# Optimization experiments

Measured on AMD Instinct MI355X. Metric: run time of the kernel, lower is better.

## Reference

```python
import jax, jax.numpy as jnp
import numpy as np

# Static config (matches init_kwargs / input_specs)
B, D, H, W, C = 1, 16, 56, 56, 128
NH = 4
WS = (8, 7, 7)            # window size (d, h, w)
SS = (4, 3, 3)            # shift size = window // 2
HID = 4 * C
L = WS[0] * WS[1] * WS[2]  # 392 tokens per window
SCALE = (C // NH) ** -0.5
TABLE = (2 * WS[0] - 1) * (2 * WS[1] - 1) * (2 * WS[2] - 1)  # 2535


def _rel_index_np(wd, wh, ww):
    # Faithful to VideoSwinWindowAttention.get_relative_position_index
    yy, zz, xx = np.meshgrid(np.arange(ww), np.arange(wd), np.arange(wh))  # 'xy'
    coords = np.stack([zz, yy, xx], axis=0).reshape(3, -1)
    rc = coords[:, :, None] - coords[:, None, :]
    rc = rc.transpose(1, 2, 0)
    z = (rc[:, :, 0] + wd - 1) * (2 * wh - 1) * (2 * ww - 1)
    x = (rc[:, :, 1] + wh - 1) * (2 * ww - 1)
    y = rc[:, :, 2] + ww - 1
    return (z + x + y).astype(np.int32)  # (L, L)


def _partition_np(x, ws):
    b, d, h, w, c = x.shape
    x = x.reshape(b, d // ws[0], ws[0], h // ws[1], ws[1], w // ws[2], ws[2], c)
    x = x.transpose(0, 1, 3, 5, 2, 4, 6, 7)
    return x.reshape(-1, ws[0] * ws[1] * ws[2], c)


def _compute_mask_np(d, h, w, ws, ss):
    img = np.zeros((1, d, h, w, 1))
    cnt = 0
    for ds in (slice(-ws[0]), slice(-ws[0], -ss[0]), slice(-ss[0], None)):
        for hs in (slice(-ws[1]), slice(-ws[1], -ss[1]), slice(-ss[1], None)):
            for wsl in (slice(-ws[2]), slice(-ws[2], -ss[2]), slice(-ss[2], None)):
                img[:, ds, hs, wsl, :] = cnt
                cnt += 1
    mw = _partition_np(img, ws)[..., 0]  # (nW, L)
    am = mw[:, None, :] - mw[:, :, None]
    return np.where(am != 0, -100.0, 0.0).astype(np.float32)  # (nW, L, L)


REL_INDEX = jnp.asarray(_rel_index_np(*WS))            # (L, L) int32
ATTN_MASK = jnp.asarray(_compute_mask_np(D, H, W, WS, SS))  # (nW, L, L)


def window_partition(x, ws):
    b, d, h, w, c = x.shape
    x = x.reshape(b, d // ws[0], ws[0], h // ws[1], ws[1], w // ws[2], ws[2], c)
    x = x.transpose(0, 1, 3, 5, 2, 4, 6, 7)
    return x.reshape(-1, ws[0] * ws[1] * ws[2], c)


def window_reverse(win, ws, b, d, h, w):
    x = win.reshape(b, d // ws[0], h // ws[1], w // ws[2], ws[0], ws[1], ws[2], -1)
    x = x.transpose(0, 1, 4, 2, 5, 3, 6, 7)
    return x.reshape(b, d, h, w, -1)


def layer_norm(x, g, b, eps=1e-5):
    m = jnp.mean(x, axis=-1, keepdims=True)
    v = jnp.mean(jnp.square(x - m), axis=-1, keepdims=True)
    return (x - m) * jax.lax.rsqrt(v + eps) * g + b


def window_attention(xw, qkv_w, qkv_b, rpb, proj_w, proj_b, mask):
    bn = xw.shape[0]
    qkv = (xw @ qkv_w + qkv_b).reshape(bn, L, 3, NH, C // NH)
    q = qkv[:, :, 0].transpose(0, 2, 1, 3) * SCALE  # (bn, NH, L, hd)
    k = qkv[:, :, 1].transpose(0, 2, 1, 3)
    v = qkv[:, :, 2].transpose(0, 2, 1, 3)
    attn = jnp.einsum('bhld,bhmd->bhlm', q, k)
    bias = rpb[REL_INDEX.reshape(-1)].reshape(L, L, NH).transpose(2, 0, 1)
    attn = attn + bias[None]
    if mask is not None:
        nw = mask.shape[0]
        attn = attn.reshape(bn // nw, nw, NH, L, L) + mask[None, :, None]
        attn = attn.reshape(bn, NH, L, L)
    attn = jax.nn.softmax(attn, axis=-1)
    out = jnp.einsum('bhlm,bhmd->bhld', attn, v)
    out = out.transpose(0, 2, 1, 3).reshape(bn, L, C)
    return out @ proj_w + proj_b


def swin_block(x, p, shift, mask):
    shortcut = x
    x = layer_norm(x, p[0], p[1])
    if shift is not None:
        x = jnp.roll(x, (-shift[0], -shift[1], -shift[2]), axis=(1, 2, 3))
    xw = window_partition(x, WS)
    xw = window_attention(xw, p[2], p[3], p[4], p[5], p[6], mask)
    x = window_reverse(xw, WS, B, D, H, W)
    if shift is not None:
        x = jnp.roll(x, shift, axis=(1, 2, 3))
    x = shortcut + x
    y = layer_norm(x, p[7], p[8])
    y = jax.nn.gelu(y @ p[9] + p[10], approximate=False) @ p[11] + p[12]
    return x + y


def setup_inputs() -> dict:
    key = jax.random.key(0)
    ks = jax.random.split(key, 8)
    s = 0.02
    return {
        'x': jax.random.normal(ks[0], (B, D, H, W, C), jnp.float32),
        'ln1_g': jnp.ones((2, C), jnp.float32),
        'ln1_b': jnp.zeros((2, C), jnp.float32),
        'qkv_w': jax.random.normal(ks[1], (2, C, 3 * C), jnp.float32) * s,
        'qkv_b': jnp.zeros((2, 3 * C), jnp.float32),
        'rpb': jax.random.normal(ks[2], (2, TABLE, NH), jnp.float32) * s,
        'proj_w': jax.random.normal(ks[3], (2, C, C), jnp.float32) * s,
        'proj_b': jnp.zeros((2, C), jnp.float32),
        'ln2_g': jnp.ones((2, C), jnp.float32),
        'ln2_b': jnp.zeros((2, C), jnp.float32),
        'fc1_w': jax.random.normal(ks[4], (2, C, HID), jnp.float32) * s,
        'fc1_b': jnp.zeros((2, HID), jnp.float32),
        'fc2_w': jax.random.normal(ks[5], (2, HID, C), jnp.float32) * s,
        'fc2_b': jnp.zeros((2, C), jnp.float32),
    }


def reference(x, ln1_g, ln1_b, qkv_w, qkv_b, rpb, proj_w, proj_b,
              ln2_g, ln2_b, fc1_w, fc1_b, fc2_w, fc2_b):
    # Block 0: W-MSA (no shift, no mask). Block 1: SW-MSA (shift + mask).
    for i, (shift, mask) in enumerate(((None, None), (SS, ATTN_MASK))):
        p = (ln1_g[i], ln1_b[i], qkv_w[i], qkv_b[i], rpb[i], proj_w[i],
             proj_b[i], ln2_g[i], ln2_b[i], fc1_w[i], fc1_b[i], fc2_w[i], fc2_b[i])
        x = swin_block(x, p, shift, mask)
    return x
```

## Files before the change

kernel.cpp:

```cpp
#include <hip/hip_runtime.h>
#include <hip/hip_bf16.h>
#include <math.h>


#define NTOK 50176
#define CC   128
#define LL   392
#define NWIN 128
#define NHEAD 4
#define HDIM 32
#define QKSCALE 0.17677669529663687f
#define LOG2E   1.4426950408889634f

#define KOFF    0
#define VOFF    12544
#define POFF    25088
#define LDS_U16 33280

#define KTILE   12544

#define KADDR(row, g) (((row) << 5) + ((((g) ^ ((row) & 3) ^ (((row) >> 2) & 3))) << 3))
#define VADDR(d, k) (VOFF + (d)*392 + (k))

#define BM_PER_HEAD (13*392*16)
#define BM_TOTAL    (8*4*BM_PER_HEAD)

typedef unsigned short u16;
typedef unsigned int   u32;
typedef unsigned long long u64;
typedef __attribute__((ext_vector_type(8))) short short8;
typedef __attribute__((ext_vector_type(4))) float f32x4;
typedef __attribute__((ext_vector_type(2))) unsigned int u32x2;
typedef __attribute__((ext_vector_type(4))) unsigned int u32x4;

#define GLDS(gp, lp) __builtin_amdgcn_global_load_lds( \
    (const __attribute__((address_space(1))) void*)(gp), \
    (__attribute__((address_space(3))) void*)(lp), 16, 0, 0)

__device__ __forceinline__ float b2f_lo(u32 u){ return __uint_as_float(u<<16); }
__device__ __forceinline__ float b2f_hi(u32 u){ return __uint_as_float(u & 0xffff0000u); }
__device__ __forceinline__ u16 f2b(float f){
  __hip_bfloat16 h = __float2bfloat16(f);
  return *reinterpret_cast<u16*>(&h);
}
__device__ __forceinline__ u32 cvtpk(float lo, float hi){
  u32 r; asm("v_cvt_pk_bf16_f32 %0, %1, %2" : "=v"(r) : "v"(lo), "v"(hi)); return r;
}

__device__ __forceinline__ int row_to_pos(int r, int shifted){
  int w = r / LL, t = r - w*LL;
  int wd = w >> 6, wh = (w >> 3) & 7, ww = w & 7;
  int td = t / 49, rem = t - td*49, th = rem / 7, tw = rem - th*7;
  int d = wd*8 + td, h = wh*7 + th, x = ww*7 + tw;
  if (shifted){ d = (d+4)&15; h += 3; if (h>=56) h-=56; x += 3; if (x>=56) x-=56; }
  return (d*56 + h)*56 + x;
}

__device__ __forceinline__ int pos_to_row_sh(int p){
  int d = p / 3136, rem = p - d*3136, h = rem / 56, x = rem - h*56;
  d = (d + 12) & 15; h -= 3; if (h < 0) h += 56; x -= 3; if (x < 0) x += 56;
  int wd = d >> 3, td = d & 7;
  int wh = h / 7, th = h - wh*7, ww = x / 7, tw = x - ww*7;
  return (wd*64 + wh*8 + ww)*LL + td*49 + th*7 + tw;
}

__global__ __launch_bounds__(256) void ln_kernel(
    const float* __restrict__ xf, const float* __restrict__ g,
    const float* __restrict__ b, u16* __restrict__ out, int do_map, int shifted)
{
  int wave = threadIdx.x >> 6, lane = threadIdx.x & 63;
  int r = blockIdx.x*4 + wave;
  int pos = do_map ? row_to_pos(r, shifted) : r;
  long src = (long)pos * CC;
  float v0 = xf[src+lane], v1 = xf[src+64+lane];
  float s = v0+v1, ss = v0*v0 + v1*v1;
  #pragma unroll
  for (int o=32; o>0; o>>=1){ s += __shfl_xor(s,o); ss += __shfl_xor(ss,o); }
  float mean = s*(1.f/CC);
  float var  = ss*(1.f/CC) - mean*mean;
  float rstd = rsqrtf(var + 1e-5f);
  long dst = (long)r*CC;
  out[dst + lane]      = f2b((v0-mean)*rstd*g[lane]    + b[lane]);
  out[dst + 64 + lane] = f2b((v1-mean)*rstd*g[64+lane] + b[64+lane]);
}

__global__ __launch_bounds__(256) void wtall_kernel(
    const float* __restrict__ qkvw, const float* __restrict__ projw,
    const float* __restrict__ fc1w, const float* __restrict__ fc2w,
    u16* __restrict__ wts)
{
  int t = blockIdx.x*256 + threadIdx.x;
  int blk = t / 196608, r = t - blk*196608;
  const float* in; int Kd, Nd, off;
  if (r < 49152)      { in = qkvw + (size_t)blk*49152; Kd = 128; Nd = 384; off = r; }
  else if (r < 65536) { in = projw + (size_t)blk*16384; Kd = 128; Nd = 128; off = r - 49152; }
  else if (r < 131072){ in = fc1w + (size_t)blk*65536;  Kd = 128; Nd = 512; off = r - 65536; }
  else                { in = fc2w + (size_t)blk*65536;  Kd = 512; Nd = 128; off = r - 131072; }
  int n = off / Kd, k = off - n*Kd;
  wts[t] = f2b(in[k*Nd + n]);
}

__global__ __launch_bounds__(256) void biasm_kernel(
    const float* __restrict__ rpb, u32* __restrict__ bm, int total)
{
  int t = blockIdx.x*256 + threadIdx.x;
  if (t >= total) return;
  int jj = t & 15; int rest = t >> 4;
  int i  = rest % 392; rest /= 392;
  int s  = rest % 13;  rest /= 13;
  int h  = rest & 3;   int cls = rest >> 2;
  int tdi=i/49, rmi=i-tdi*49, thi=rmi/7, twi=rmi-thi*7;
  u32 pack = 0;
  #pragma unroll
  for (int half=0; half<2; half++){
    int j = s*32 + jj + half*16;
    float v = -1e30f;
    if (j < LL){
      int tdj=j/49, rmj=j-tdj*49, thj=rmj/7, twj=rmj-thj*7;
      int idx = (tdi-tdj)*169 + (thi-thj)*13 + (twi-twj) + 1267;
      v = rpb[idx*NHEAD + h];
      bool neq = ((cls&4) && ((tdi<4) != (tdj<4)))
              || ((cls&2) && ((thi<4) != (thj<4)))
              || ((cls&1) && ((twi<4) != (twj<4)));
      if (neq) v -= 100.f;
      v *= LOG2E;
    }
    pack |= ((u32)f2b(v)) << (16*half);
  }
  bm[t] = pack;
}

template<int KD, int EPI, int LNF, int NW>
__global__ __launch_bounds__(NW*64) void mm_kernel(
    const u16* __restrict__ A, const u16* __restrict__ Wt, int ldw,
    const float* __restrict__ bias, u16* __restrict__ OutB, int ldo,
    float* __restrict__ OutF, const float* __restrict__ Res,
    const float* __restrict__ lng, const float* __restrict__ lnb,
    float scaleq, int shifted, int use_bias)
{
  constexpr int NCH  = NW/2;
  constexpr int COLW = 128/NCH;
  constexpr int CT   = COLW/16;
  constexpr bool SWAPG = (EPI == 0);

  __shared__ __align__(16) u16 As[2*128*32];
  __shared__ __align__(16) u16 Bs[2*128*32];
  const int tid = threadIdx.x, lane = tid & 63, wv = tid >> 6;
  const int quad = lane >> 4, l15 = lane & 15;
  const int rh = wv / NCH, ch = wv % NCH;
  const int r0 = (SWAPG ? blockIdx.y : blockIdx.x) * 128;
  const int n0 = (SWAPG ? blockIdx.x : blockIdx.y) * 128;
  const int srow = lane >> 2, spart = (lane & 3) * 8;
  const int nkt = KD/32;

  f32x4 acc[4][CT] = {};

  auto stage = [&](int kt, int bo){
    const int k0 = kt*32;
    #pragma unroll
    for (int t=0;t<8/NW;t++){
      const int rowbase = (wv*(8/NW) + t)*16;
      GLDS(&A [(long)(r0 + rowbase + srow)*KD  + k0 + spart], &As[bo + rowbase*32]);
      GLDS(&Wt[(long)(n0 + rowbase + srow)*ldw + k0 + spart], &Bs[bo + rowbase*32]);
    }
  };
  auto compute = [&](int bo){
    short8 af[4], bf[CT];
    #pragma unroll
    for (int rt=0;rt<4;rt++)
      af[rt] = *reinterpret_cast<const short8*>(&As[bo + (rh*64 + rt*16 + l15)*32 + quad*8]);
    #pragma unroll
    for (int ct=0;ct<CT;ct++)
      bf[ct] = *reinterpret_cast<const short8*>(&Bs[bo + (ch*COLW + ct*16 + l15)*32 + quad*8]);
    #pragma unroll
    for (int rt=0;rt<4;rt++)
      #pragma unroll
      for (int ct=0;ct<CT;ct++)
        acc[rt][ct] = __builtin_amdgcn_mfma_f32_16x16x32_bf16(af[rt], bf[ct], acc[rt][ct], 0,0,0);
  };

  stage(0, 0);
  asm volatile("s_waitcnt vmcnt(0)" ::: "memory");
  __builtin_amdgcn_s_barrier();

  int cur = 0;
  for (int kt = 0; kt < nkt-1; kt++){
    stage(kt+1, 4096 - cur);
    compute(cur);
    asm volatile("s_waitcnt vmcnt(0)" ::: "memory");
    __builtin_amdgcn_s_barrier();
    cur = 4096 - cur;
  }
  compute(cur);

  if (EPI == 0){
    const int y = n0 >> 7;
    if (y == 0){
      #pragma unroll
      for (int rt=0;rt<4;rt++)
        #pragma unroll
        for (int rr=0;rr<4;rr++){
          const int row_g = r0 + rh*64 + rt*16 + quad*4 + rr;
          #pragma unroll
          for (int ct=0;ct<CT;ct++){
            const int c = ch*COLW + ct*16 + l15;
            float v = (acc[rt][ct][rr] + bias[c]) * scaleq;
            OutB[(long)row_g*128 + c] = f2b(v);
          }
        }
    } else if (y == 1){
      u16* Kreg = OutB + (size_t)NTOK*128;
      #pragma unroll
      for (int rt=0;rt<4;rt++)
        #pragma unroll
        for (int rr=0;rr<4;rr++){
          const int row_g = r0 + rh*64 + rt*16 + quad*4 + rr;
          const int wi = row_g / 392, key = row_g - wi*392;
          #pragma unroll
          for (int ct=0;ct<CT;ct++){
            const int c = ch*COLW + ct*16 + l15;
            const int hd = c >> 5, d = c & 31;
            float v = acc[rt][ct][rr] + bias[128 + c];
            Kreg[(size_t)(wi*4 + hd)*KTILE + KADDR(key, d>>3) + (d&7)] = f2b(v);
          }
        }
    } else {
      u16* Vreg = OutB + (size_t)NTOK*256;
      #pragma unroll
      for (int rt=0;rt<4;rt++){
        const int rbase = r0 + rh*64 + rt*16 + quad*4;
        const int wi = rbase / 392, key0 = rbase - wi*392;
        #pragma unroll
        for (int ct=0;ct<CT;ct++){
          const int c = ch*COLW + ct*16 + l15;
          const int hd = c >> 5, d = c & 31;
          const float bb = bias[256 + c];
          u32 lo = cvtpk(acc[rt][ct][0] + bb, acc[rt][ct][1] + bb);
          u32 hi = cvtpk(acc[rt][ct][2] + bb, acc[rt][ct][3] + bb);
          u64 pk = (u64)lo | ((u64)hi << 32);
          *reinterpret_cast<u64*>(&Vreg[(size_t)(wi*4 + hd)*KTILE + (size_t)d*392 + key0]) = pk;
        }
      }
    }
  } else if (LNF == 0){
    #pragma unroll
    for (int rt=0;rt<4;rt++){
      #pragma unroll
      for (int rr=0;rr<4;rr++){
        const int row_g = r0 + rh*64 + rt*16 + quad*4 + rr;
        long pos = 0;
        if (EPI == 2) pos = (long)row_to_pos(row_g, shifted) * CC;
        #pragma unroll
        for (int ct=0;ct<CT;ct++){
          const int col_g = n0 + ch*COLW + ct*16 + l15;
          float v = acc[rt][ct][rr];
          if (EPI == 1){
            v += bias[col_g];
            v = 0.5f*v*(1.f + erff(v*0.70710678118654752f));
            OutB[(long)row_g*ldo + col_g] = f2b(v);
          } else if (EPI == 2){
            OutF[pos + col_g] = Res[pos + col_g] + v + bias[col_g];
          } else {
            float o = OutF[(long)row_g*CC + col_g] + v;
            if (use_bias) o += bias[col_g];
            OutF[(long)row_g*CC + col_g] = o;
          }
        }
      }
    }
  } else {
    float* red = (float*)As;
    int pose[4][4];
    #pragma unroll
    for (int rt=0;rt<4;rt++){
      #pragma unroll
      for (int rr=0;rr<4;rr++){
        const int row_g = r0 + rh*64 + rt*16 + quad*4 + rr;
        int pos = (EPI == 2) ? row_to_pos(row_g, shifted) : row_g;
        pose[rt][rr] = pos;
        long pb = (long)pos * CC;
        float s = 0.f, ss = 0.f;
        #pragma unroll
        for (int ct=0;ct<CT;ct++){
          const int col_g = n0 + ch*COLW + ct*16 + l15;
          float v = acc[rt][ct][rr];
          float o;
          if (EPI == 2) o = Res[pb + col_g] + v + bias[col_g];
          else { o = OutF[pb + col_g] + v; if (use_bias) o += bias[col_g]; }
          OutF[pb + col_g] = o;
          acc[rt][ct][rr] = o;
          s += o; ss += o*o;
        }
        #pragma unroll
        for (int off=1; off<16; off<<=1){
          s  += __shfl_xor(s,  off);
          ss += __shfl_xor(ss, off);
        }
        if (l15 == 0){
          int rl = rh*64 + rt*16 + quad*4 + rr;
          red[rl*(2*NCH) + ch*2]     = s;
          red[rl*(2*NCH) + ch*2 + 1] = ss;
        }
      }
    }
    __syncthreads();
    #pragma unroll
    for (int rt=0;rt<4;rt++){
      #pragma unroll
      for (int rr=0;rr<4;rr++){
        const int rl = rh*64 + rt*16 + quad*4 + rr;
        float st = 0.f, sst = 0.f;
        #pragma unroll
        for (int j=0;j<NCH;j++){
          st  += red[rl*(2*NCH) + j*2];
          sst += red[rl*(2*NCH) + j*2 + 1];
        }
        float mean = st*(1.f/128.f);
        float var  = sst*(1.f/128.f) - mean*mean;
        float rstd = rsqrtf(var + 1e-5f);
        long oidx;
        if (LNF == 1) oidx = (long)pose[rt][rr] * CC;
        else          oidx = (long)pos_to_row_sh(pose[rt][rr]) * CC;
        #pragma unroll
        for (int ct=0;ct<CT;ct++){
          const int col_g = n0 + ch*COLW + ct*16 + l15;
          float val = (acc[rt][ct][rr] - mean)*rstd*lng[col_g] + lnb[col_g];
          OutB[oidx + col_g] = f2b(val);
        }
      }
    }
  }
}

__global__ __launch_bounds__(512, 4) void attn_kernel(
    const u16* __restrict__ qkv, const u32* __restrict__ bm,
    u16* __restrict__ out, int shifted)
{
  __shared__ __align__(16) u16 lds[LDS_U16];

  const int w = blockIdx.x >> 2, head = blockIdx.x & 3;
  const int tid = threadIdx.x, lane = tid & 63, wave = tid >> 6;
  const int quad = lane >> 4, l15 = lane & 15;
  const int wd = w>>6, wh = (w>>3)&7, ww = w&7;
  const int cls = shifted ? (((wd!=0)?4:0) | ((wh==7)?2:0) | ((ww==7)?1:0)) : 0;
  const u32* __restrict__ bmh = bm + (size_t)(cls*NHEAD + head)*BM_PER_HEAD;
  const int pbase = POFF + wave*1024;
  const int swz = l15 & 7;
  const int prow = pbase + l15*64;
  const int q2 = quad >> 1, qh = (quad & 1) << 2;

  {
    const u16* Kg = qkv + (size_t)NTOK*128 + (size_t)(w*4+head)*KTILE;
    const u16* Vg = qkv + (size_t)NTOK*256 + (size_t)(w*4+head)*KTILE;
    #pragma unroll
    for (int n = 0; n < 3; n++){
      GLDS(Kg + n*4096 + wave*512 + (lane<<3), &lds[KOFF + n*4096 + wave*512]);
      GLDS(Vg + n*4096 + wave*512 + (lane<<3), &lds[VOFF + n*4096 + wave*512]);
    }
    if (tid < 32){
      GLDS(Kg + 12288 + (lane<<3), &lds[KOFF + 12288]);
      GLDS(Vg + 12288 + (lane<<3), &lds[VOFF + 12288]);
    }
  }
  __syncthreads();

  for (int qt = wave; qt < 25; qt += 8){
    int iq = qt*16 + l15; if (iq > LL-1) iq = LL-1;
    short8 qf = *reinterpret_cast<const short8*>(
        &qkv[((size_t)(w*LL + iq))*128 + head*HDIM + quad*8]);

    float ls = 0.f;
    f32x4 oc0 = {0.f,0.f,0.f,0.f}, oc1 = {0.f,0.f,0.f,0.f};

    const int bmrow = iq*16 + quad*4;
    u32x4 bmA = *reinterpret_cast<const u32x4*>(&bmh[bmrow]);
    u32x4 bmB = *reinterpret_cast<const u32x4*>(&bmh[392*16 + bmrow]);
    short8 kf0 = *reinterpret_cast<const short8*>(&lds[KOFF + KADDR(     l15, quad)]);
    short8 kf1 = *reinterpret_cast<const short8*>(&lds[KOFF + KADDR(16 + l15, quad)]);
    short8 kf2 = *reinterpret_cast<const short8*>(&lds[KOFF + KADDR(32 + l15, quad)]);
    short8 kf3 = *reinterpret_cast<const short8*>(&lds[KOFF + KADDR(48 + l15, quad)]);

    for (int it = 0; it < 6; it++){
      const int kb = it*64;
      u32x4 bmAn = {}, bmBn = {};
      short8 kn0 = {}, kn1 = {}, kn2 = {}, kn3 = {};
      if (it < 5){
        bmAn = *reinterpret_cast<const u32x4*>(&bmh[(2*it+2)*392*16 + bmrow]);
        bmBn = *reinterpret_cast<const u32x4*>(&bmh[(2*it+3)*392*16 + bmrow]);
        kn0 = *reinterpret_cast<const short8*>(&lds[KOFF + KADDR(kb + 64 + l15, quad)]);
        kn1 = *reinterpret_cast<const short8*>(&lds[KOFF + KADDR(kb + 80 + l15, quad)]);
        kn2 = *reinterpret_cast<const short8*>(&lds[KOFF + KADDR(kb + 96 + l15, quad)]);
        kn3 = *reinterpret_cast<const short8*>(&lds[KOFF + KADDR(kb +112 + l15, quad)]);
      } else {
        bmAn = *reinterpret_cast<const u32x4*>(&bmh[12*392*16 + bmrow]);
        kn0 = *reinterpret_cast<const short8*>(&lds[KOFF + KADDR(384 + (l15 & 7), quad)]);
        kn1 = kn0;
      }

      f32x4 z = {0.f,0.f,0.f,0.f};
      __builtin_amdgcn_s_setprio(1);
      f32x4 c0 = __builtin_amdgcn_mfma_f32_16x16x32_bf16(kf0, qf, z, 0,0,0);
      f32x4 c1 = __builtin_amdgcn_mfma_f32_16x16x32_bf16(kf1, qf, z, 0,0,0);
      f32x4 c2 = __builtin_amdgcn_mfma_f32_16x16x32_bf16(kf2, qf, z, 0,0,0);
      f32x4 c3 = __builtin_amdgcn_mfma_f32_16x16x32_bf16(kf3, qf, z, 0,0,0);
      __builtin_amdgcn_s_setprio(0);

      float p0[4], p1[4], p2[4], p3[4];
      #pragma unroll
      for (int r=0;r<4;r++){
        p0[r] = exp2f(c0[r] + b2f_lo(bmA[r]));
        p1[r] = exp2f(c1[r] + b2f_hi(bmA[r]));
        p2[r] = exp2f(c2[r] + b2f_lo(bmB[r]));
        p3[r] = exp2f(c3[r] + b2f_hi(bmB[r]));
        ls += (p0[r] + p1[r]) + (p2[r] + p3[r]);
      }

      u32x2 w0, w1, w2, w3;
      w0.x = cvtpk(p0[0], p0[1]); w0.y = cvtpk(p0[2], p0[3]);
      w1.x = cvtpk(p1[0], p1[1]); w1.y = cvtpk(p1[2], p1[3]);
      w2.x = cvtpk(p2[0], p2[1]); w2.y = cvtpk(p2[2], p2[3]);
      w3.x = cvtpk(p3[0], p3[1]); w3.y = cvtpk(p3[2], p3[3]);
      *reinterpret_cast<u32x2*>(&lds[prow + (((0 + q2) ^ swz) << 3) + qh]) = w0;
      *reinterpret_cast<u32x2*>(&lds[prow + (((2 + q2) ^ swz) << 3) + qh]) = w1;
      *reinterpret_cast<u32x2*>(&lds[prow + (((4 + q2) ^ swz) << 3) + qh]) = w2;
      *reinterpret_cast<u32x2*>(&lds[prow + (((6 + q2) ^ swz) << 3) + qh]) = w3;

      short8 pa0 = *reinterpret_cast<const short8*>(&lds[prow + (((quad    ) ^ swz) << 3)]);
      short8 pa1 = *reinterpret_cast<const short8*>(&lds[prow + (((quad + 4) ^ swz) << 3)]);
      short8 vb00 = *reinterpret_cast<const short8*>(&lds[VADDR(     l15, kb      + quad*8)]);
      short8 vb01 = *reinterpret_cast<const short8*>(&lds[VADDR(16 + l15, kb      + quad*8)]);
      short8 vb10 = *reinterpret_cast<const short8*>(&lds[VADDR(     l15, kb + 32 + quad*8)]);
      short8 vb11 = *reinterpret_cast<const short8*>(&lds[VADDR(16 + l15, kb + 32 + quad*8)]);
      __builtin_amdgcn_s_setprio(1);
      oc0 = __builtin_amdgcn_mfma_f32_16x16x32_bf16(pa0, vb00, oc0, 0,0,0);
      oc1 = __builtin_amdgcn_mfma_f32_16x16x32_bf16(pa0, vb01, oc1, 0,0,0);
      oc0 = __builtin_amdgcn_mfma_f32_16x16x32_bf16(pa1, vb10, oc0, 0,0,0);
      oc1 = __builtin_amdgcn_mfma_f32_16x16x32_bf16(pa1, vb11, oc1, 0,0,0);
      __builtin_amdgcn_s_setprio(0);

      bmA = bmAn; bmB = bmBn;
      kf0 = kn0; kf1 = kn1; kf2 = kn2; kf3 = kn3;
    }

    {
      f32x4 z = {0.f,0.f,0.f,0.f};
      f32x4 c0 = __builtin_amdgcn_mfma_f32_16x16x32_bf16(kf0, qf, z, 0,0,0);
      f32x4 c1 = __builtin_amdgcn_mfma_f32_16x16x32_bf16(kf1, qf, z, 0,0,0);
      float p0[4], p1[4];
      #pragma unroll
      for (int r=0;r<4;r++){
        p0[r] = exp2f(c0[r] + b2f_lo(bmA[r]));
        p1[r] = exp2f(c1[r] + b2f_hi(bmA[r]));
        ls += p0[r] + p1[r];
      }
      u32x2 w0, w1;
      w0.x = cvtpk(p0[0], p0[1]); w0.y = cvtpk(p0[2], p0[3]);
      w1.x = cvtpk(p1[0], p1[1]); w1.y = cvtpk(p1[2], p1[3]);
      *reinterpret_cast<u32x2*>(&lds[prow + (((0 + q2) ^ swz) << 3) + qh]) = w0;
      *reinterpret_cast<u32x2*>(&lds[prow + (((2 + q2) ^ swz) << 3) + qh]) = w1;
      short8 pa0 = *reinterpret_cast<const short8*>(&lds[prow + ((quad ^ swz) << 3)]);
      short8 vb0 = *reinterpret_cast<const short8*>(&lds[VADDR(     l15, 384)]);
      short8 vb1 = *reinterpret_cast<const short8*>(&lds[VADDR(16 + l15, 384)]);
      oc0 = __builtin_amdgcn_mfma_f32_16x16x32_bf16(pa0, vb0, oc0, 0,0,0);
      oc1 = __builtin_amdgcn_mfma_f32_16x16x32_bf16(pa0, vb1, oc1, 0,0,0);
    }

    ls += __shfl_xor(ls, 16);
    ls += __shfl_xor(ls, 32);
    float inv = 1.f / ls;
    #pragma unroll
    for (int r=0;r<4;r++){
      float invr = __shfl(inv, quad*4 + r);
      int i = qt*16 + quad*4 + r;
      if (i < LL){
        long o = ((long)(w*LL + i))*CC + head*HDIM;
        out[o + l15]      = f2b(oc0[r]*invr);
        out[o + 16 + l15] = f2b(oc1[r]*invr);
      }
    }
  }
}

extern "C" void kernel_launch(void* const* d_in, const int* in_sizes, int n_in,
                              void* d_out, int out_size, void* d_ws, size_t ws_size,
                              hipStream_t stream)
{
  const float* x     = (const float*)d_in[0];
  const float* ln1g  = (const float*)d_in[1];
  const float* ln1b  = (const float*)d_in[2];
  const float* qkvw  = (const float*)d_in[3];
  const float* qkvb  = (const float*)d_in[4];
  const float* rpb   = (const float*)d_in[5];
  const float* projw = (const float*)d_in[6];
  const float* projb = (const float*)d_in[7];
  const float* ln2g  = (const float*)d_in[8];
  const float* ln2b  = (const float*)d_in[9];
  const float* fc1w  = (const float*)d_in[10];
  const float* fc1b  = (const float*)d_in[11];
  const float* fc2w  = (const float*)d_in[12];
  const float* fc2b  = (const float*)d_in[13];
  float* outf = (float*)d_out;

  u16* buf1 = (u16*)d_ws;
  u16* bufq = buf1 + (size_t)NTOK*CC;
  u16* ln2o = bufq + (size_t)NTOK*256;
  u16* hid  = bufq + (size_t)NTOK*384;
  u16* wts  = hid  + (size_t)NTOK*512;
  u32* bm   = (u32*)(wts + 393216);

  wtall_kernel<<<1536, 256, 0, stream>>>(qkvw, projw, fc1w, fc2w, wts);

  for (int blk = 0; blk < 2; ++blk){
    const int sh = blk;
    const float* resid = (blk==0) ? x : outf;
    u16* wb = wts + (size_t)blk*196608;

    const int bmtot = (blk==0) ? 4*BM_PER_HEAD : BM_TOTAL;
    biasm_kernel<<<(bmtot+255)/256, 256, 0, stream>>>(
        rpb + (size_t)blk*2535*NHEAD, bm, bmtot);
    if (blk == 0)
      ln_kernel<<<NTOK/4, 256, 0, stream>>>(resid,
          ln1g, ln1b, buf1, 1, 0);
    mm_kernel<128,0,0,4><<<dim3(3,392), 256, 0, stream>>>(
        buf1, wb, 128, qkvb + blk*384, bufq, 128,
        nullptr, nullptr, nullptr, nullptr, QKSCALE*LOG2E, 0, 0);
    attn_kernel<<<NWIN*NHEAD, 512, 0, stream>>>(bufq, bm, buf1, sh);
    mm_kernel<128,2,1,8><<<dim3(392,1), 512, 0, stream>>>(
        buf1, wb+49152, 128, projb + blk*CC, ln2o, 0,
        outf, resid, ln2g + blk*CC, ln2b + blk*CC, 1.f, sh, 0);
    mm_kernel<128,1,0,8><<<dim3(392,4), 512, 0, stream>>>(
        ln2o, wb + 65536, 128,
        fc1b + blk*512, hid, 512,
        nullptr, nullptr, nullptr, nullptr, 1.f, 0, 0);
    if (blk == 0){
      mm_kernel<512,3,2,8><<<dim3(392,1), 512, 0, stream>>>(
          hid, wb + 131072, 512,
          fc2b, buf1, 0,
          outf, nullptr, ln1g + CC, ln1b + CC, 1.f, 0, 1);
    } else {
      mm_kernel<512,3,0,8><<<dim3(392,1), 512, 0, stream>>>(
          hid, wb + 131072, 512,
          fc2b + CC, nullptr, 0,
          outf, nullptr, nullptr, nullptr, 1.f, 0, 1);
    }
  }
}
```

Before: 380.8 us.

## Deepen GEMM prefetch pipeline and fold attention bias into MFMA accumulator

The GEMM kernel now takes a template buffer count (3 or 4) and prefetches up to two K-tiles ahead. It waits with partial vmcnt values, so later tiles' global-to-LDS loads keep running while the current tile is computed, instead of waiting for all loads at every step. In the attention kernel, the combined bias/mask values now seed the QK^T MFMA accumulator rather than being added before exp2, which removes the per-element adds. The price is more LDS per GEMM block, which may lower occupancy, and a little more register setup for the bias vectors.

```diff
diff --git a/kernel.cpp b/kernel.cpp
--- a/kernel.cpp
+++ b/kernel.cpp
@@ -130,7 +130,7 @@
   bm[t] = pack;
 }
 
-template<int KD, int EPI, int LNF, int NW>
+template<int KD, int EPI, int LNF, int NW, int NBUF>
 __global__ __launch_bounds__(NW*64) void mm_kernel(
     const u16* __restrict__ A, const u16* __restrict__ Wt, int ldw,
     const float* __restrict__ bias, u16* __restrict__ OutB, int ldo,
@@ -142,9 +142,11 @@
   constexpr int COLW = 128/NCH;
   constexpr int CT   = COLW/16;
   constexpr bool SWAPG = (EPI == 0);
-
-  __shared__ __align__(16) u16 As[2*128*32];
-  __shared__ __align__(16) u16 Bs[2*128*32];
+  constexpr int LPS = 16/NW;
+  constexpr int LA  = NBUF - 2;
+
+  __shared__ __align__(16) u16 As[NBUF*128*32];
+  __shared__ __align__(16) u16 Bs[NBUF*128*32];
   const int tid = threadIdx.x, lane = tid & 63, wv = tid >> 6;
   const int quad = lane >> 4, l15 = lane & 15;
   const int rh = wv / NCH, ch = wv % NCH;
@@ -155,7 +157,8 @@
 
   f32x4 acc[4][CT] = {};
 
-  auto stage = [&](int kt, int bo){
+  auto stage = [&](int kt){
+    const int bo = (kt % NBUF) * 4096;
     const int k0 = kt*32;
     #pragma unroll
     for (int t=0;t<8/NW;t++){
@@ -164,7 +167,8 @@
       GLDS(&Wt[(long)(n0 + rowbase + srow)*ldw + k0 + spart], &Bs[bo + rowbase*32]);
     }
   };
-  auto compute = [&](int bo){
+  auto compute = [&](int kt){
+    const int bo = (kt % NBUF) * 4096;
     short8 af[4], bf[CT];
     #pragma unroll
     for (int rt=0;rt<4;rt++)
@@ -179,19 +183,21 @@
         acc[rt][ct] = __builtin_amdgcn_mfma_f32_16x16x32_bf16(af[rt], bf[ct], acc[rt][ct], 0,0,0);
   };
 
-  stage(0, 0);
-  asm volatile("s_waitcnt vmcnt(0)" ::: "memory");
-  __builtin_amdgcn_s_barrier();
-
-  int cur = 0;
-  for (int kt = 0; kt < nkt-1; kt++){
-    stage(kt+1, 4096 - cur);
-    compute(cur);
-    asm volatile("s_waitcnt vmcnt(0)" ::: "memory");
+  #pragma unroll
+  for (int p = 0; p < LA; p++) stage(p);
+
+  for (int kt = 0; kt < nkt; kt++){
+    if (kt + LA < nkt) stage(kt + LA);
+    const int rem = nkt - 1 - kt;
+    const int ahead = rem < LA ? rem : LA;
+    const int allow = ahead * LPS;
+    if (allow == 0)      asm volatile("s_waitcnt vmcnt(0)" ::: "memory");
+    else if (allow == 2) asm volatile("s_waitcnt vmcnt(2)" ::: "memory");
+    else if (allow == 4) asm volatile("s_waitcnt vmcnt(4)" ::: "memory");
+    else                 asm volatile("s_waitcnt vmcnt(8)" ::: "memory");
     __builtin_amdgcn_s_barrier();
-    cur = 4096 - cur;
+    compute(kt);
   }
-  compute(cur);
 
   if (EPI == 0){
     const int y = n0 >> 7;
@@ -397,21 +403,24 @@
         kn1 = kn0;
       }
 
-      f32x4 z = {0.f,0.f,0.f,0.f};
+      f32x4 cb0 = {b2f_lo(bmA[0]), b2f_lo(bmA[1]), b2f_lo(bmA[2]), b2f_lo(bmA[3])};
+      f32x4 cb1 = {b2f_hi(bmA[0]), b2f_hi(bmA[1]), b2f_hi(bmA[2]), b2f_hi(bmA[3])};
+      f32x4 cb2 = {b2f_lo(bmB[0]), b2f_lo(bmB[1]), b2f_lo(bmB[2]), b2f_lo(bmB[3])};
+      f32x4 cb3 = {b2f_hi(bmB[0]), b2f_hi(bmB[1]), b2f_hi(bmB[2]), b2f_hi(bmB[3])};
       __builtin_amdgcn_s_setprio(1);
-      f32x4 c0 = __builtin_amdgcn_mfma_f32_16x16x32_bf16(kf0, qf, z, 0,0,0);
-      f32x4 c1 = __builtin_amdgcn_mfma_f32_16x16x32_bf16(kf1, qf, z, 0,0,0);
-      f32x4 c2 = __builtin_amdgcn_mfma_f32_16x16x32_bf16(kf2, qf, z, 0,0,0);
-      f32x4 c3 = __builtin_amdgcn_mfma_f32_16x16x32_bf16(kf3, qf, z, 0,0,0);
+      f32x4 c0 = __builtin_amdgcn_mfma_f32_16x16x32_bf16(kf0, qf, cb0, 0,0,0);
+      f32x4 c1 = __builtin_amdgcn_mfma_f32_16x16x32_bf16(kf1, qf, cb1, 0,0,0);
+      f32x4 c2 = __builtin_amdgcn_mfma_f32_16x16x32_bf16(kf2, qf, cb2, 0,0,0);
+      f32x4 c3 = __builtin_amdgcn_mfma_f32_16x16x32_bf16(kf3, qf, cb3, 0,0,0);
       __builtin_amdgcn_s_setprio(0);
 
       float p0[4], p1[4], p2[4], p3[4];
       #pragma unroll
       for (int r=0;r<4;r++){
-        p0[r] = exp2f(c0[r] + b2f_lo(bmA[r]));
-        p1[r] = exp2f(c1[r] + b2f_hi(bmA[r]));
-        p2[r] = exp2f(c2[r] + b2f_lo(bmB[r]));
-        p3[r] = exp2f(c3[r] + b2f_hi(bmB[r]));
+        p0[r] = exp2f(c0[r]);
+        p1[r] = exp2f(c1[r]);
+        p2[r] = exp2f(c2[r]);
+        p3[r] = exp2f(c3[r]);
         ls += (p0[r] + p1[r]) + (p2[r] + p3[r]);
       }
 
@@ -443,14 +452,15 @@
     }
 
     {
-      f32x4 z = {0.f,0.f,0.f,0.f};
-      f32x4 c0 = __builtin_amdgcn_mfma_f32_16x16x32_bf16(kf0, qf, z, 0,0,0);
-      f32x4 c1 = __builtin_amdgcn_mfma_f32_16x16x32_bf16(kf1, qf, z, 0,0,0);
+      f32x4 cb0 = {b2f_lo(bmA[0]), b2f_lo(bmA[1]), b2f_lo(bmA[2]), b2f_lo(bmA[3])};
+      f32x4 cb1 = {b2f_hi(bmA[0]), b2f_hi(bmA[1]), b2f_hi(bmA[2]), b2f_hi(bmA[3])};
+      f32x4 c0 = __builtin_amdgcn_mfma_f32_16x16x32_bf16(kf0, qf, cb0, 0,0,0);
+      f32x4 c1 = __builtin_amdgcn_mfma_f32_16x16x32_bf16(kf1, qf, cb1, 0,0,0);
       float p0[4], p1[4];
       #pragma unroll
       for (int r=0;r<4;r++){
-        p0[r] = exp2f(c0[r] + b2f_lo(bmA[r]));
-        p1[r] = exp2f(c1[r] + b2f_hi(bmA[r]));
+        p0[r] = exp2f(c0[r]);
+        p1[r] = exp2f(c1[r]);
         ls += p0[r] + p1[r];
       }
       u32x2 w0, w1;
@@ -521,24 +531,24 @@
     if (blk == 0)
       ln_kernel<<<NTOK/4, 256, 0, stream>>>(resid,
           ln1g, ln1b, buf1, 1, 0);
-    mm_kernel<128,0,0,4><<<dim3(3,392), 256, 0, stream>>>(
+    mm_kernel<128,0,0,4,3><<<dim3(3,392), 256, 0, stream>>>(
         buf1, wb, 128, qkvb + blk*384, bufq, 128,
         nullptr, nullptr, nullptr, nullptr, QKSCALE*LOG2E, 0, 0);
     attn_kernel<<<NWIN*NHEAD, 512, 0, stream>>>(bufq, bm, buf1, sh);
-    mm_kernel<128,2,1,8><<<dim3(392,1), 512, 0, stream>>>(
+    mm_kernel<128,2,1,8,4><<<dim3(392,1), 512, 0, stream>>>(
         buf1, wb+49152, 128, projb + blk*CC, ln2o, 0,
         outf, resid, ln2g + blk*CC, ln2b + blk*CC, 1.f, sh, 0);
-    mm_kernel<128,1,0,8><<<dim3(392,4), 512, 0, stream>>>(
+    mm_kernel<128,1,0,8,3><<<dim3(392,4), 512, 0, stream>>>(
         ln2o, wb + 65536, 128,
         fc1b + blk*512, hid, 512,
         nullptr, nullptr, nullptr, nullptr, 1.f, 0, 0);
     if (blk == 0){
-      mm_kernel<512,3,2,8><<<dim3(392,1), 512, 0, stream>>>(
+      mm_kernel<512,3,2,8,4><<<dim3(392,1), 512, 0, stream>>>(
           hid, wb + 131072, 512,
           fc2b, buf1, 0,
           outf, nullptr, ln1g + CC, ln1b + CC, 1.f, 0, 1);
     } else {
-      mm_kernel<512,3,0,8><<<dim3(392,1), 512, 0, stream>>>(
+      mm_kernel<512,3,0,8,4><<<dim3(392,1), 512, 0, stream>>>(
           hid, wb + 131072, 512,
           fc2b + CC, nullptr, 0,
           outf, nullptr, nullptr, nullptr, 1.f, 0, 1);
```

Result: no change. 383.9 us (+0.8%).
